# Kernel tuning notes

Measured on AMD Instinct MI355X. Metric: run time of the kernel, lower is better.

## Reference

```python
import jax, jax.numpy as jnp
import numpy as np

GROUP_SIZE = 64


def _ternary_ste(w):
    # bf16 group-wise ternary quantization with straight-through estimator
    wb = w.astype(jnp.bfloat16)
    w_g = wb.reshape(-1, GROUP_SIZE)
    scale = jnp.clip(jnp.mean(jnp.abs(w_g), axis=-1, keepdims=True), 1e-8, None)
    q = (jnp.clip(jnp.round(w_g / scale), -1, 1) * scale).reshape(wb.shape)
    # forward value = q, gradient flows through wb (bf16 cast of w)
    return wb + jax.lax.stop_gradient(q - wb)


def setup_inputs() -> dict:
    key = jax.random.key(0)
    k_x, k_f, k_p = jax.random.split(key, 3)
    N, in_f, out_f, num_f = 16384, 1024, 4096, 16
    x = jax.random.normal(k_x, (N, in_f), dtype=jnp.float32)
    features = jax.random.uniform(k_f, (num_f, in_f), minval=-0.02, maxval=0.02, dtype=jnp.float32)
    prototypes = jax.random.uniform(k_p, (out_f, in_f), minval=-0.02, maxval=0.02, dtype=jnp.float32)
    theta = jnp.float32(1.0)
    alpha = jnp.float32(0.5)
    beta = jnp.float32(0.5)
    return {"x": x, "features": features, "prototypes": prototypes,
            "theta": theta, "alpha": alpha, "beta": beta}


def reference(x, features, prototypes, theta, alpha, beta):
    # low-rank feature projections (K = num_features = 16)
    x_f = x @ features.T                                   # [N, 16]
    p_q = _ternary_ste(prototypes).astype(jnp.float32)     # [out, in]
    p_f = p_q @ features.T                                 # [out, 16]
    x_s = jax.nn.sigmoid(x_f * 5.0)
    p_s = jax.nn.sigmoid(p_f * 5.0)
    x_a = x_f * x_s
    p_a = p_f * p_s
    return (jnp.abs(theta) * (x_a @ p_a.T)
            - jnp.abs(alpha) * (x_a @ (1.0 - p_s).T)
            - jnp.abs(beta) * ((1.0 - x_s) @ p_a.T))
```

## Files before the change

### kernel.cpp

```cpp
#include <hip/hip_runtime.h>
#include <hip/hip_bf16.h>
#include <math.h>

#define NF     16
#define INF    1024
#define NPROTO 4096
#define NROWS  16384

typedef __attribute__((ext_vector_type(8))) short short8;
typedef __attribute__((ext_vector_type(4))) float f32x4;
typedef __attribute__((ext_vector_type(2))) float f32x2;

__device__ __forceinline__ float bf16_rne(float x) {
    unsigned u = __float_as_uint(x);
    unsigned r = (u + 0x7FFFu + ((u >> 16) & 1u)) & 0xFFFF0000u;
    return __uint_as_float(r);
}
__device__ __forceinline__ unsigned short bf16_hi(float v) {
    unsigned u = __float_as_uint(v);
    return (unsigned short)((u + 0x7FFFu + ((u >> 16) & 1u)) >> 16);
}
__device__ __forceinline__ void split_bf16(float v, unsigned short& hi, unsigned short& lo) {
    unsigned u  = __float_as_uint(v);
    unsigned r  = u + 0x7FFFu + ((u >> 16) & 1u);
    hi = (unsigned short)(r >> 16);
    float hf = __uint_as_float(r & 0xFFFF0000u);
    lo = bf16_hi(v - hf);
}
__device__ __forceinline__ float sigmoid5(float z) {
    return 1.0f / (1.0f + __expf(-5.0f * z));
}

__global__ __launch_bounds__(256) void bfrag_kernel(
    const float* __restrict__ feat,
    unsigned short* __restrict__ BFh, unsigned short* __restrict__ BFl)
{
    const int t = blockIdx.x * 256 + threadIdx.x;
    const int kstep = t >> 6, lane = t & 63;
    const int n = lane & 15, b = lane >> 4;
    const float* src = feat + (size_t)n * INF + kstep * 32 + b * 8;
    float4 v0 = *(const float4*)(src);
    float4 v1 = *(const float4*)(src + 4);
    unsigned short h[8], l[8];
    split_bf16(v0.x, h[0], l[0]); split_bf16(v0.y, h[1], l[1]);
    split_bf16(v0.z, h[2], l[2]); split_bf16(v0.w, h[3], l[3]);
    split_bf16(v1.x, h[4], l[4]); split_bf16(v1.y, h[5], l[5]);
    split_bf16(v1.z, h[6], l[6]); split_bf16(v1.w, h[7], l[7]);
#pragma unroll
    for (int e = 0; e < 8; ++e) { BFh[t * 8 + e] = h[e]; BFl[t * 8 + e] = l[e]; }
}

__global__ __launch_bounds__(256, 4) void prep(
    const float* __restrict__ x, const float* __restrict__ proto,
    const float* __restrict__ theta, const float* __restrict__ alpha,
    const float* __restrict__ beta,
    const unsigned short* __restrict__ BFh, const unsigned short* __restrict__ BFl,
    unsigned short* __restrict__ Ph, unsigned short* __restrict__ Pl,
    unsigned short* __restrict__ Xh, unsigned short* __restrict__ Xl)
{
    __shared__ f32x4 red[4][64];
    const int lane = threadIdx.x & 63;
    const int w    = threadIdx.x >> 6;
    const int m = lane & 15, b = lane >> 4;
    const int blk = blockIdx.x;
    const bool is_pe = (blk < NPROTO / 16);
    const int rowbase = (is_pe ? blk : blk - NPROTO / 16) * 16;
    const float* rowp = (is_pe ? proto : x) + (size_t)(rowbase + m) * INF;

    f32x4 acc = {0.f, 0.f, 0.f, 0.f};

    if (is_pe) {
#pragma unroll
        for (int gi = 0; gi < 4; ++gi) {
            const int g = w * 4 + gi;
            const float* pg = rowp + g * 64 + b * 8;
            float4 v0 = *(const float4*)(pg);
            float4 v1 = *(const float4*)(pg + 4);
            float4 v2 = *(const float4*)(pg + 32);
            float4 v3 = *(const float4*)(pg + 36);
            float w0 = bf16_rne(v0.x), w1 = bf16_rne(v0.y), w2 = bf16_rne(v0.z), w3 = bf16_rne(v0.w);
            float w4 = bf16_rne(v1.x), w5 = bf16_rne(v1.y), w6 = bf16_rne(v1.z), w7 = bf16_rne(v1.w);
            float w8 = bf16_rne(v2.x), w9 = bf16_rne(v2.y), wa = bf16_rne(v2.z), wb = bf16_rne(v2.w);
            float wc = bf16_rne(v3.x), wd = bf16_rne(v3.y), we = bf16_rne(v3.z), wf = bf16_rne(v3.w);
            float p0 = ((fabsf(w0) + fabsf(w1)) + fabsf(w2)) + fabsf(w3);
            float p1 = ((fabsf(w4) + fabsf(w5)) + fabsf(w6)) + fabsf(w7);
            float p2 = ((fabsf(w8) + fabsf(w9)) + fabsf(wa)) + fabsf(wb);
            float p3 = ((fabsf(wc) + fabsf(wd)) + fabsf(we)) + fabsf(wf);
            float p = ((p0 + p1) + p2) + p3;
            p += __shfl_xor(p, 16, 64);
            p += __shfl_xor(p, 32, 64);
            float scale = fmaxf(bf16_rne(p * (1.0f / 64.0f)), 1e-8f);
            float inv = 1.0f / scale;
            short8 A0, A1;
            A0[0] = (short)bf16_hi(fminf(fmaxf(rintf(bf16_rne(w0 * inv)), -1.f), 1.f) * scale);
            A0[1] = (short)bf16_hi(fminf(fmaxf(rintf(bf16_rne(w1 * inv)), -1.f), 1.f) * scale);
            A0[2] = (short)bf16_hi(fminf(fmaxf(rintf(bf16_rne(w2 * inv)), -1.f), 1.f) * scale);
            A0[3] = (short)bf16_hi(fminf(fmaxf(rintf(bf16_rne(w3 * inv)), -1.f), 1.f) * scale);
            A0[4] = (short)bf16_hi(fminf(fmaxf(rintf(bf16_rne(w4 * inv)), -1.f), 1.f) * scale);
            A0[5] = (short)bf16_hi(fminf(fmaxf(rintf(bf16_rne(w5 * inv)), -1.f), 1.f) * scale);
            A0[6] = (short)bf16_hi(fminf(fmaxf(rintf(bf16_rne(w6 * inv)), -1.f), 1.f) * scale);
            A0[7] = (short)bf16_hi(fminf(fmaxf(rintf(bf16_rne(w7 * inv)), -1.f), 1.f) * scale);
            A1[0] = (short)bf16_hi(fminf(fmaxf(rintf(bf16_rne(w8 * inv)), -1.f), 1.f) * scale);
            A1[1] = (short)bf16_hi(fminf(fmaxf(rintf(bf16_rne(w9 * inv)), -1.f), 1.f) * scale);
            A1[2] = (short)bf16_hi(fminf(fmaxf(rintf(bf16_rne(wa * inv)), -1.f), 1.f) * scale);
            A1[3] = (short)bf16_hi(fminf(fmaxf(rintf(bf16_rne(wb * inv)), -1.f), 1.f) * scale);
            A1[4] = (short)bf16_hi(fminf(fmaxf(rintf(bf16_rne(wc * inv)), -1.f), 1.f) * scale);
            A1[5] = (short)bf16_hi(fminf(fmaxf(rintf(bf16_rne(wd * inv)), -1.f), 1.f) * scale);
            A1[6] = (short)bf16_hi(fminf(fmaxf(rintf(bf16_rne(we * inv)), -1.f), 1.f) * scale);
            A1[7] = (short)bf16_hi(fminf(fmaxf(rintf(bf16_rne(wf * inv)), -1.f), 1.f) * scale);
            const short8 Bh0 = *(const short8*)(BFh + ((size_t)(2 * g) * 64 + lane) * 8);
            const short8 Bl0 = *(const short8*)(BFl + ((size_t)(2 * g) * 64 + lane) * 8);
            const short8 Bh1 = *(const short8*)(BFh + ((size_t)(2 * g + 1) * 64 + lane) * 8);
            const short8 Bl1 = *(const short8*)(BFl + ((size_t)(2 * g + 1) * 64 + lane) * 8);
            acc = __builtin_amdgcn_mfma_f32_16x16x32_bf16(A0, Bh0, acc, 0, 0, 0);
            acc = __builtin_amdgcn_mfma_f32_16x16x32_bf16(A0, Bl0, acc, 0, 0, 0);
            acc = __builtin_amdgcn_mfma_f32_16x16x32_bf16(A1, Bh1, acc, 0, 0, 0);
            acc = __builtin_amdgcn_mfma_f32_16x16x32_bf16(A1, Bl1, acc, 0, 0, 0);
        }
    } else {
#pragma unroll
        for (int ki = 0; ki < 8; ++ki) {
            const int kstep = w * 8 + ki;
            const float* pk = rowp + kstep * 32 + b * 8;
            float4 v0 = *(const float4*)(pk);
            float4 v1 = *(const float4*)(pk + 4);
            unsigned short h0,l0,h1,l1,h2,l2,h3,l3,h4,l4,h5,l5,h6,l6,h7,l7;
            split_bf16(v0.x, h0, l0); split_bf16(v0.y, h1, l1);
            split_bf16(v0.z, h2, l2); split_bf16(v0.w, h3, l3);
            split_bf16(v1.x, h4, l4); split_bf16(v1.y, h5, l5);
            split_bf16(v1.z, h6, l6); split_bf16(v1.w, h7, l7);
            short8 Ah, Al;
            Ah[0]=(short)h0; Ah[1]=(short)h1; Ah[2]=(short)h2; Ah[3]=(short)h3;
            Ah[4]=(short)h4; Ah[5]=(short)h5; Ah[6]=(short)h6; Ah[7]=(short)h7;
            Al[0]=(short)l0; Al[1]=(short)l1; Al[2]=(short)l2; Al[3]=(short)l3;
            Al[4]=(short)l4; Al[5]=(short)l5; Al[6]=(short)l6; Al[7]=(short)l7;
            const short8 Bh = *(const short8*)(BFh + ((size_t)kstep * 64 + lane) * 8);
            const short8 Bl = *(const short8*)(BFl + ((size_t)kstep * 64 + lane) * 8);
            acc = __builtin_amdgcn_mfma_f32_16x16x32_bf16(Ah, Bh, acc, 0, 0, 0);
            acc = __builtin_amdgcn_mfma_f32_16x16x32_bf16(Ah, Bl, acc, 0, 0, 0);
            acc = __builtin_amdgcn_mfma_f32_16x16x32_bf16(Al, Bh, acc, 0, 0, 0);
            acc = __builtin_amdgcn_mfma_f32_16x16x32_bf16(Al, Bl, acc, 0, 0, 0);
        }
    }

    red[w][lane] = acc;
    __syncthreads();
    if (w == 0) {
        f32x4 a0 = red[0][lane], a1 = red[1][lane], a2 = red[2][lane], a3 = red[3][lane];
        f32x4 tot = (a0 + a1) + (a2 + a3);
        if (is_pe) {
            const float th = fabsf(theta[0]);
            const float al = fabsf(alpha[0]);
            const float be = fabsf(beta[0]);
#pragma unroll
            for (int reg = 0; reg < 4; ++reg) {
                const int row = rowbase + b * 4 + reg;
                float pf = tot[reg];
                float ps = sigmoid5(pf);
                float pa = pf * ps;
                unsigned short h0,l0,h1,l1;
                split_bf16(th * pa - al * (1.0f - ps), h0, l0);
                split_bf16(-be * pa, h1, l1);
                Ph[row * 32 + m]      = h0;  Pl[row * 32 + m]      = l0;
                Ph[row * 32 + 16 + m] = h1;  Pl[row * 32 + 16 + m] = l1;
            }
        } else {
#pragma unroll
            for (int reg = 0; reg < 4; ++reg) {
                const int row = rowbase + b * 4 + reg;
                float xf = tot[reg];
                float xs = sigmoid5(xf);
                unsigned short h0,l0,h1,l1;
                split_bf16(xf * xs, h0, l0);
                split_bf16(1.0f - xs, h1, l1);
                Xh[row * 32 + m]      = h0;  Xl[row * 32 + m]      = l0;
                Xh[row * 32 + 16 + m] = h1;  Xl[row * 32 + 16 + m] = l1;
            }
        }
    }
}

__global__ __launch_bounds__(64) void main_mm_mfma(
    const unsigned short* __restrict__ Xh, const unsigned short* __restrict__ Xl,
    const unsigned short* __restrict__ Ph,
    float* __restrict__ out)
{
    __shared__ float lds[16][128];
    const int lane  = threadIdx.x & 63;
    const int m     = lane & 15;
    const int b     = lane >> 4;
    const int nbase = blockIdx.y * 16;
    const int ob    = blockIdx.x * 128;

    const size_t boff = (size_t)(nbase + m) * 32 + b * 8;
    const short8 Bh = *(const short8*)(Xh + boff);
    const short8 Bl = *(const short8*)(Xl + boff);

    const int wsw = 4 * (m & 7);
    float* myrow = &lds[m][0];
#pragma unroll
    for (int t = 0; t < 8; ++t) {
        const size_t aoff = (size_t)(ob + t * 16 + m) * 32 + b * 8;
        const short8 Ah = *(const short8*)(Ph + aoff);
        f32x4 acc = {0.f, 0.f, 0.f, 0.f};
        acc = __builtin_amdgcn_mfma_f32_16x16x32_bf16(Ah, Bh, acc, 0, 0, 0);
        acc = __builtin_amdgcn_mfma_f32_16x16x32_bf16(Ah, Bl, acc, 0, 0, 0);
        *(f32x4*)(myrow + ((t * 16 + b * 4) ^ wsw)) = acc;
    }

    const float* src = &lds[0][0];
#pragma unroll
    for (int r = 0; r < 16; ++r) {
        f32x2 v = *(const f32x2*)(src + r * 128 + ((lane * 2) ^ (4 * (r & 7))));
        f32x2* dst = (f32x2*)(out + (size_t)(nbase + r) * NPROTO + ob + lane * 2);
        __builtin_nontemporal_store(v, dst);
    }
}

extern "C" void kernel_launch(void* const* d_in, const int* in_sizes, int n_in,
                              void* d_out, int out_size, void* d_ws, size_t ws_size,
                              hipStream_t stream) {
    const float* x     = (const float*)d_in[0];
    const float* feat  = (const float*)d_in[1];
    const float* proto = (const float*)d_in[2];
    const float* theta = (const float*)d_in[3];
    const float* alpha = (const float*)d_in[4];
    const float* beta  = (const float*)d_in[5];
    float* out = (float*)d_out;

    unsigned short* Ph  = (unsigned short*)d_ws;
    unsigned short* Pl  = Ph + (size_t)NPROTO * 32;
    unsigned short* Xh  = Pl + (size_t)NPROTO * 32;
    unsigned short* Xl  = Xh + (size_t)NROWS * 32;
    unsigned short* BFh = Xl + (size_t)NROWS * 32;
    unsigned short* BFl = BFh + (size_t)2048 * 8;

    bfrag_kernel<<<dim3(8), 256, 0, stream>>>(feat, BFh, BFl);
    prep<<<dim3(NPROTO / 16 + NROWS / 16), 256, 0, stream>>>(
        x, proto, theta, alpha, beta, BFh, BFl, Ph, Pl, Xh, Xl);
    main_mm_mfma<<<dim3(NPROTO / 128, NROWS / 16), 64, 0, stream>>>(Xh, Xl, Ph, out);
}
```

Baseline: 69.68 us.

## Fuse x-feature projection into main matmul kernel and split prototype prep

Prototype prep now runs in its own kernel, and the x projection (x@features with hi/lo bf16 split plus sigmoid activation) moves into the main output kernel. The per-row X fragments are staged in LDS instead of going through global workspace. Each 256-thread block then produces a 16x4096 output strip, with its four waves each covering 1024 columns. This removes the Xh/Xl global round trip and one dispatch, at the cost of fewer blocks (1024) each doing much more serial work and using more LDS. The Pl buffer is also dropped, since the main matmul never read it.

```diff
diff --git a/kernel.cpp b/kernel.cpp
--- a/kernel.cpp
+++ b/kernel.cpp
@@ -50,97 +50,67 @@
     for (int e = 0; e < 8; ++e) { BFh[t * 8 + e] = h[e]; BFl[t * 8 + e] = l[e]; }
 }
 
-__global__ __launch_bounds__(256, 4) void prep(
-    const float* __restrict__ x, const float* __restrict__ proto,
+__global__ __launch_bounds__(256, 4) void prep_pe(
+    const float* __restrict__ proto,
     const float* __restrict__ theta, const float* __restrict__ alpha,
     const float* __restrict__ beta,
     const unsigned short* __restrict__ BFh, const unsigned short* __restrict__ BFl,
-    unsigned short* __restrict__ Ph, unsigned short* __restrict__ Pl,
-    unsigned short* __restrict__ Xh, unsigned short* __restrict__ Xl)
+    unsigned short* __restrict__ Ph)
 {
     __shared__ f32x4 red[4][64];
     const int lane = threadIdx.x & 63;
     const int w    = threadIdx.x >> 6;
     const int m = lane & 15, b = lane >> 4;
-    const int blk = blockIdx.x;
-    const bool is_pe = (blk < NPROTO / 16);
-    const int rowbase = (is_pe ? blk : blk - NPROTO / 16) * 16;
-    const float* rowp = (is_pe ? proto : x) + (size_t)(rowbase + m) * INF;
+    const int rowbase = blockIdx.x * 16;
+    const float* rowp = proto + (size_t)(rowbase + m) * INF;
 
     f32x4 acc = {0.f, 0.f, 0.f, 0.f};
-
-    if (is_pe) {
-#pragma unroll
-        for (int gi = 0; gi < 4; ++gi) {
-            const int g = w * 4 + gi;
-            const float* pg = rowp + g * 64 + b * 8;
-            float4 v0 = *(const float4*)(pg);
-            float4 v1 = *(const float4*)(pg + 4);
-            float4 v2 = *(const float4*)(pg + 32);
-            float4 v3 = *(const float4*)(pg + 36);
-            float w0 = bf16_rne(v0.x), w1 = bf16_rne(v0.y), w2 = bf16_rne(v0.z), w3 = bf16_rne(v0.w);
-            float w4 = bf16_rne(v1.x), w5 = bf16_rne(v1.y), w6 = bf16_rne(v1.z), w7 = bf16_rne(v1.w);
-            float w8 = bf16_rne(v2.x), w9 = bf16_rne(v2.y), wa = bf16_rne(v2.z), wb = bf16_rne(v2.w);
-            float wc = bf16_rne(v3.x), wd = bf16_rne(v3.y), we = bf16_rne(v3.z), wf = bf16_rne(v3.w);
-            float p0 = ((fabsf(w0) + fabsf(w1)) + fabsf(w2)) + fabsf(w3);
-            float p1 = ((fabsf(w4) + fabsf(w5)) + fabsf(w6)) + fabsf(w7);
-            float p2 = ((fabsf(w8) + fabsf(w9)) + fabsf(wa)) + fabsf(wb);
-            float p3 = ((fabsf(wc) + fabsf(wd)) + fabsf(we)) + fabsf(wf);
-            float p = ((p0 + p1) + p2) + p3;
-            p += __shfl_xor(p, 16, 64);
-            p += __shfl_xor(p, 32, 64);
-            float scale = fmaxf(bf16_rne(p * (1.0f / 64.0f)), 1e-8f);
-            float inv = 1.0f / scale;
-            short8 A0, A1;
-            A0[0] = (short)bf16_hi(fminf(fmaxf(rintf(bf16_rne(w0 * inv)), -1.f), 1.f) * scale);
-            A0[1] = (short)bf16_hi(fminf(fmaxf(rintf(bf16_rne(w1 * inv)), -1.f), 1.f) * scale);
-            A0[2] = (short)bf16_hi(fminf(fmaxf(rintf(bf16_rne(w2 * inv)), -1.f), 1.f) * scale);
-            A0[3] = (short)bf16_hi(fminf(fmaxf(rintf(bf16_rne(w3 * inv)), -1.f), 1.f) * scale);
-            A0[4] = (short)bf16_hi(fminf(fmaxf(rintf(bf16_rne(w4 * inv)), -1.f), 1.f) * scale);
-            A0[5] = (short)bf16_hi(fminf(fmaxf(rintf(bf16_rne(w5 * inv)), -1.f), 1.f) * scale);
-            A0[6] = (short)bf16_hi(fminf(fmaxf(rintf(bf16_rne(w6 * inv)), -1.f), 1.f) * scale);
-            A0[7] = (short)bf16_hi(fminf(fmaxf(rintf(bf16_rne(w7 * inv)), -1.f), 1.f) * scale);
-            A1[0] = (short)bf16_hi(fminf(fmaxf(rintf(bf16_rne(w8 * inv)), -1.f), 1.f) * scale);
-            A1[1] = (short)bf16_hi(fminf(fmaxf(rintf(bf16_rne(w9 * inv)), -1.f), 1.f) * scale);
-            A1[2] = (short)bf16_hi(fminf(fmaxf(rintf(bf16_rne(wa * inv)), -1.f), 1.f) * scale);
-            A1[3] = (short)bf16_hi(fminf(fmaxf(rintf(bf16_rne(wb * inv)), -1.f), 1.f) * scale);
-            A1[4] = (short)bf16_hi(fminf(fmaxf(rintf(bf16_rne(wc * inv)), -1.f), 1.f) * scale);
-            A1[5] = (short)bf16_hi(fminf(fmaxf(rintf(bf16_rne(wd * inv)), -1.f), 1.f) * scale);
-            A1[6] = (short)bf16_hi(fminf(fmaxf(rintf(bf16_rne(we * inv)), -1.f), 1.f) * scale);
-            A1[7] = (short)bf16_hi(fminf(fmaxf(rintf(bf16_rne(wf * inv)), -1.f), 1.f) * scale);
-            const short8 Bh0 = *(const short8*)(BFh + ((size_t)(2 * g) * 64 + lane) * 8);
-            const short8 Bl0 = *(const short8*)(BFl + ((size_t)(2 * g) * 64 + lane) * 8);
-            const short8 Bh1 = *(const short8*)(BFh + ((size_t)(2 * g + 1) * 64 + lane) * 8);
-            const short8 Bl1 = *(const short8*)(BFl + ((size_t)(2 * g + 1) * 64 + lane) * 8);
-            acc = __builtin_amdgcn_mfma_f32_16x16x32_bf16(A0, Bh0, acc, 0, 0, 0);
-            acc = __builtin_amdgcn_mfma_f32_16x16x32_bf16(A0, Bl0, acc, 0, 0, 0);
-            acc = __builtin_amdgcn_mfma_f32_16x16x32_bf16(A1, Bh1, acc, 0, 0, 0);
-            acc = __builtin_amdgcn_mfma_f32_16x16x32_bf16(A1, Bl1, acc, 0, 0, 0);
-        }
-    } else {
-#pragma unroll
-        for (int ki = 0; ki < 8; ++ki) {
-            const int kstep = w * 8 + ki;
-            const float* pk = rowp + kstep * 32 + b * 8;
-            float4 v0 = *(const float4*)(pk);
-            float4 v1 = *(const float4*)(pk + 4);
-            unsigned short h0,l0,h1,l1,h2,l2,h3,l3,h4,l4,h5,l5,h6,l6,h7,l7;
-            split_bf16(v0.x, h0, l0); split_bf16(v0.y, h1, l1);
-            split_bf16(v0.z, h2, l2); split_bf16(v0.w, h3, l3);
-            split_bf16(v1.x, h4, l4); split_bf16(v1.y, h5, l5);
-            split_bf16(v1.z, h6, l6); split_bf16(v1.w, h7, l7);
-            short8 Ah, Al;
-            Ah[0]=(short)h0; Ah[1]=(short)h1; Ah[2]=(short)h2; Ah[3]=(short)h3;
-            Ah[4]=(short)h4; Ah[5]=(short)h5; Ah[6]=(short)h6; Ah[7]=(short)h7;
-            Al[0]=(short)l0; Al[1]=(short)l1; Al[2]=(short)l2; Al[3]=(short)l3;
-            Al[4]=(short)l4; Al[5]=(short)l5; Al[6]=(short)l6; Al[7]=(short)l7;
-            const short8 Bh = *(const short8*)(BFh + ((size_t)kstep * 64 + lane) * 8);
-            const short8 Bl = *(const short8*)(BFl + ((size_t)kstep * 64 + lane) * 8);
-            acc = __builtin_amdgcn_mfma_f32_16x16x32_bf16(Ah, Bh, acc, 0, 0, 0);
-            acc = __builtin_amdgcn_mfma_f32_16x16x32_bf16(Ah, Bl, acc, 0, 0, 0);
-            acc = __builtin_amdgcn_mfma_f32_16x16x32_bf16(Al, Bh, acc, 0, 0, 0);
-            acc = __builtin_amdgcn_mfma_f32_16x16x32_bf16(Al, Bl, acc, 0, 0, 0);
-        }
+#pragma unroll
+    for (int gi = 0; gi < 4; ++gi) {
+        const int g = w * 4 + gi;
+        const float* pg = rowp + g * 64 + b * 8;
+        float4 v0 = *(const float4*)(pg);
+        float4 v1 = *(const float4*)(pg + 4);
+        float4 v2 = *(const float4*)(pg + 32);
+        float4 v3 = *(const float4*)(pg + 36);
+        float w0 = bf16_rne(v0.x), w1 = bf16_rne(v0.y), w2 = bf16_rne(v0.z), w3 = bf16_rne(v0.w);
+        float w4 = bf16_rne(v1.x), w5 = bf16_rne(v1.y), w6 = bf16_rne(v1.z), w7 = bf16_rne(v1.w);
+        float w8 = bf16_rne(v2.x), w9 = bf16_rne(v2.y), wa = bf16_rne(v2.z), wb = bf16_rne(v2.w);
+        float wc = bf16_rne(v3.x), wd = bf16_rne(v3.y), we = bf16_rne(v3.z), wf = bf16_rne(v3.w);
+        float p0 = ((fabsf(w0) + fabsf(w1)) + fabsf(w2)) + fabsf(w3);
+        float p1 = ((fabsf(w4) + fabsf(w5)) + fabsf(w6)) + fabsf(w7);
+        float p2 = ((fabsf(w8) + fabsf(w9)) + fabsf(wa)) + fabsf(wb);
+        float p3 = ((fabsf(wc) + fabsf(wd)) + fabsf(we)) + fabsf(wf);
+        float p = ((p0 + p1) + p2) + p3;
+        p += __shfl_xor(p, 16, 64);
+        p += __shfl_xor(p, 32, 64);
+        float scale = fmaxf(bf16_rne(p * (1.0f / 64.0f)), 1e-8f);
+        float inv = 1.0f / scale;
+        short8 A0, A1;
+        A0[0] = (short)bf16_hi(fminf(fmaxf(rintf(bf16_rne(w0 * inv)), -1.f), 1.f) * scale);
+        A0[1] = (short)bf16_hi(fminf(fmaxf(rintf(bf16_rne(w1 * inv)), -1.f), 1.f) * scale);
+        A0[2] = (short)bf16_hi(fminf(fmaxf(rintf(bf16_rne(w2 * inv)), -1.f), 1.f) * scale);
+        A0[3] = (short)bf16_hi(fminf(fmaxf(rintf(bf16_rne(w3 * inv)), -1.f), 1.f) * scale);
+        A0[4] = (short)bf16_hi(fminf(fmaxf(rintf(bf16_rne(w4 * inv)), -1.f), 1.f) * scale);
+        A0[5] = (short)bf16_hi(fminf(fmaxf(rintf(bf16_rne(w5 * inv)), -1.f), 1.f) * scale);
+        A0[6] = (short)bf16_hi(fminf(fmaxf(rintf(bf16_rne(w6 * inv)), -1.f), 1.f) * scale);
+        A0[7] = (short)bf16_hi(fminf(fmaxf(rintf(bf16_rne(w7 * inv)), -1.f), 1.f) * scale);
+        A1[0] = (short)bf16_hi(fminf(fmaxf(rintf(bf16_rne(w8 * inv)), -1.f), 1.f) * scale);
+        A1[1] = (short)bf16_hi(fminf(fmaxf(rintf(bf16_rne(w9 * inv)), -1.f), 1.f) * scale);
+        A1[2] = (short)bf16_hi(fminf(fmaxf(rintf(bf16_rne(wa * inv)), -1.f), 1.f) * scale);
+        A1[3] = (short)bf16_hi(fminf(fmaxf(rintf(bf16_rne(wb * inv)), -1.f), 1.f) * scale);
+        A1[4] = (short)bf16_hi(fminf(fmaxf(rintf(bf16_rne(wc * inv)), -1.f), 1.f) * scale);
+        A1[5] = (short)bf16_hi(fminf(fmaxf(rintf(bf16_rne(wd * inv)), -1.f), 1.f) * scale);
+        A1[6] = (short)bf16_hi(fminf(fmaxf(rintf(bf16_rne(we * inv)), -1.f), 1.f) * scale);
+        A1[7] = (short)bf16_hi(fminf(fmaxf(rintf(bf16_rne(wf * inv)), -1.f), 1.f) * scale);
+        const short8 Bh0 = *(const short8*)(BFh + ((size_t)(2 * g) * 64 + lane) * 8);
+        const short8 Bl0 = *(const short8*)(BFl + ((size_t)(2 * g) * 64 + lane) * 8);
+        const short8 Bh1 = *(const short8*)(BFh + ((size_t)(2 * g + 1) * 64 + lane) * 8);
+        const short8 Bl1 = *(const short8*)(BFl + ((size_t)(2 * g + 1) * 64 + lane) * 8);
+        acc = __builtin_amdgcn_mfma_f32_16x16x32_bf16(A0, Bh0, acc, 0, 0, 0);
+        acc = __builtin_amdgcn_mfma_f32_16x16x32_bf16(A0, Bl0, acc, 0, 0, 0);
+        acc = __builtin_amdgcn_mfma_f32_16x16x32_bf16(A1, Bh1, acc, 0, 0, 0);
+        acc = __builtin_amdgcn_mfma_f32_16x16x32_bf16(A1, Bl1, acc, 0, 0, 0);
     }
 
     red[w][lane] = acc;
@@ -148,72 +118,104 @@
     if (w == 0) {
         f32x4 a0 = red[0][lane], a1 = red[1][lane], a2 = red[2][lane], a3 = red[3][lane];
         f32x4 tot = (a0 + a1) + (a2 + a3);
-        if (is_pe) {
-            const float th = fabsf(theta[0]);
-            const float al = fabsf(alpha[0]);
-            const float be = fabsf(beta[0]);
-#pragma unroll
-            for (int reg = 0; reg < 4; ++reg) {
-                const int row = rowbase + b * 4 + reg;
-                float pf = tot[reg];
-                float ps = sigmoid5(pf);
-                float pa = pf * ps;
-                unsigned short h0,l0,h1,l1;
-                split_bf16(th * pa - al * (1.0f - ps), h0, l0);
-                split_bf16(-be * pa, h1, l1);
-                Ph[row * 32 + m]      = h0;  Pl[row * 32 + m]      = l0;
-                Ph[row * 32 + 16 + m] = h1;  Pl[row * 32 + 16 + m] = l1;
-            }
-        } else {
-#pragma unroll
-            for (int reg = 0; reg < 4; ++reg) {
-                const int row = rowbase + b * 4 + reg;
-                float xf = tot[reg];
-                float xs = sigmoid5(xf);
-                unsigned short h0,l0,h1,l1;
-                split_bf16(xf * xs, h0, l0);
-                split_bf16(1.0f - xs, h1, l1);
-                Xh[row * 32 + m]      = h0;  Xl[row * 32 + m]      = l0;
-                Xh[row * 32 + 16 + m] = h1;  Xl[row * 32 + 16 + m] = l1;
-            }
-        }
-    }
-}
-
-__global__ __launch_bounds__(64) void main_mm_mfma(
-    const unsigned short* __restrict__ Xh, const unsigned short* __restrict__ Xl,
+        const float th = fabsf(theta[0]);
+        const float al = fabsf(alpha[0]);
+        const float be = fabsf(beta[0]);
+#pragma unroll
+        for (int reg = 0; reg < 4; ++reg) {
+            const int row = rowbase + b * 4 + reg;
+            float pf = tot[reg];
+            float ps = sigmoid5(pf);
+            float pa = pf * ps;
+            Ph[row * 32 + m]      = bf16_hi(th * pa - al * (1.0f - ps));
+            Ph[row * 32 + 16 + m] = bf16_hi(-be * pa);
+        }
+    }
+}
+
+__global__ __launch_bounds__(256, 4) void fused_main(
+    const float* __restrict__ x,
+    const unsigned short* __restrict__ BFh, const unsigned short* __restrict__ BFl,
     const unsigned short* __restrict__ Ph,
     float* __restrict__ out)
 {
-    __shared__ float lds[16][128];
-    const int lane  = threadIdx.x & 63;
-    const int m     = lane & 15;
-    const int b     = lane >> 4;
-    const int nbase = blockIdx.y * 16;
-    const int ob    = blockIdx.x * 128;
-
-    const size_t boff = (size_t)(nbase + m) * 32 + b * 8;
-    const short8 Bh = *(const short8*)(Xh + boff);
-    const short8 Bl = *(const short8*)(Xl + boff);
-
-    const int wsw = 4 * (m & 7);
-    float* myrow = &lds[m][0];
-#pragma unroll
-    for (int t = 0; t < 8; ++t) {
-        const size_t aoff = (size_t)(ob + t * 16 + m) * 32 + b * 8;
-        const short8 Ah = *(const short8*)(Ph + aoff);
-        f32x4 acc = {0.f, 0.f, 0.f, 0.f};
+    __shared__ float ldsT[4][16][128];
+    __shared__ f32x4 red[4][64];
+    __shared__ unsigned short XeH[16][32], XeL[16][32];
+
+    const int lane = threadIdx.x & 63;
+    const int w    = threadIdx.x >> 6;
+    const int m = lane & 15, b = lane >> 4;
+    const int rowbase = blockIdx.x * 16;
+    const float* rowp = x + (size_t)(rowbase + m) * INF;
+
+    f32x4 acc = {0.f, 0.f, 0.f, 0.f};
+#pragma unroll
+    for (int ki = 0; ki < 8; ++ki) {
+        const int kstep = w * 8 + ki;
+        const float* pk = rowp + kstep * 32 + b * 8;
+        float4 v0 = *(const float4*)(pk);
+        float4 v1 = *(const float4*)(pk + 4);
+        unsigned short h0,l0,h1,l1,h2,l2,h3,l3,h4,l4,h5,l5,h6,l6,h7,l7;
+        split_bf16(v0.x, h0, l0); split_bf16(v0.y, h1, l1);
+        split_bf16(v0.z, h2, l2); split_bf16(v0.w, h3, l3);
+        split_bf16(v1.x, h4, l4); split_bf16(v1.y, h5, l5);
+        split_bf16(v1.z, h6, l6); split_bf16(v1.w, h7, l7);
+        short8 Ah, Al;
+        Ah[0]=(short)h0; Ah[1]=(short)h1; Ah[2]=(short)h2; Ah[3]=(short)h3;
+        Ah[4]=(short)h4; Ah[5]=(short)h5; Ah[6]=(short)h6; Ah[7]=(short)h7;
+        Al[0]=(short)l0; Al[1]=(short)l1; Al[2]=(short)l2; Al[3]=(short)l3;
+        Al[4]=(short)l4; Al[5]=(short)l5; Al[6]=(short)l6; Al[7]=(short)l7;
+        const short8 Bh = *(const short8*)(BFh + ((size_t)kstep * 64 + lane) * 8);
+        const short8 Bl = *(const short8*)(BFl + ((size_t)kstep * 64 + lane) * 8);
         acc = __builtin_amdgcn_mfma_f32_16x16x32_bf16(Ah, Bh, acc, 0, 0, 0);
         acc = __builtin_amdgcn_mfma_f32_16x16x32_bf16(Ah, Bl, acc, 0, 0, 0);
-        *(f32x4*)(myrow + ((t * 16 + b * 4) ^ wsw)) = acc;
-    }
-
-    const float* src = &lds[0][0];
-#pragma unroll
-    for (int r = 0; r < 16; ++r) {
-        f32x2 v = *(const f32x2*)(src + r * 128 + ((lane * 2) ^ (4 * (r & 7))));
-        f32x2* dst = (f32x2*)(out + (size_t)(nbase + r) * NPROTO + ob + lane * 2);
-        __builtin_nontemporal_store(v, dst);
+        acc = __builtin_amdgcn_mfma_f32_16x16x32_bf16(Al, Bh, acc, 0, 0, 0);
+        acc = __builtin_amdgcn_mfma_f32_16x16x32_bf16(Al, Bl, acc, 0, 0, 0);
+    }
+    red[w][lane] = acc;
+    __syncthreads();
+    if (w == 0) {
+        f32x4 a0 = red[0][lane], a1 = red[1][lane], a2 = red[2][lane], a3 = red[3][lane];
+        f32x4 tot = (a0 + a1) + (a2 + a3);
+#pragma unroll
+        for (int reg = 0; reg < 4; ++reg) {
+            const int row = b * 4 + reg;
+            float xf = tot[reg];
+            float xs = sigmoid5(xf);
+            unsigned short h0,l0,h1,l1;
+            split_bf16(xf * xs, h0, l0);
+            split_bf16(1.0f - xs, h1, l1);
+            XeH[row][m]      = h0;  XeL[row][m]      = l0;
+            XeH[row][16 + m] = h1;  XeL[row][16 + m] = l1;
+        }
+    }
+    __syncthreads();
+
+    const short8 Bh = *(const short8*)&XeH[m][b * 8];
+    const short8 Bl = *(const short8*)&XeL[m][b * 8];
+    const int wsw = 4 * (m & 7);
+    float* myrow = &ldsT[w][m][0];
+    const float* src = &ldsT[w][0][0];
+
+#pragma unroll 1
+    for (int c = 0; c < 8; ++c) {
+        const int ob = w * 1024 + c * 128;
+#pragma unroll
+        for (int t = 0; t < 8; ++t) {
+            const size_t aoff = (size_t)(ob + t * 16 + m) * 32 + b * 8;
+            const short8 Ah = *(const short8*)(Ph + aoff);
+            f32x4 a2 = {0.f, 0.f, 0.f, 0.f};
+            a2 = __builtin_amdgcn_mfma_f32_16x16x32_bf16(Ah, Bh, a2, 0, 0, 0);
+            a2 = __builtin_amdgcn_mfma_f32_16x16x32_bf16(Ah, Bl, a2, 0, 0, 0);
+            *(f32x4*)(myrow + ((t * 16 + b * 4) ^ wsw)) = a2;
+        }
+#pragma unroll
+        for (int r = 0; r < 16; ++r) {
+            f32x2 v = *(const f32x2*)(src + r * 128 + ((lane * 2) ^ (4 * (r & 7))));
+            f32x2* dst = (f32x2*)(out + (size_t)(rowbase + r) * NPROTO + ob + lane * 2);
+            __builtin_nontemporal_store(v, dst);
+        }
     }
 }
 
@@ -229,14 +231,10 @@
     float* out = (float*)d_out;
 
     unsigned short* Ph  = (unsigned short*)d_ws;
-    unsigned short* Pl  = Ph + (size_t)NPROTO * 32;
-    unsigned short* Xh  = Pl + (size_t)NPROTO * 32;
-    unsigned short* Xl  = Xh + (size_t)NROWS * 32;
-    unsigned short* BFh = Xl + (size_t)NROWS * 32;
+    unsigned short* BFh = Ph + (size_t)NPROTO * 32;
     unsigned short* BFl = BFh + (size_t)2048 * 8;
 
     bfrag_kernel<<<dim3(8), 256, 0, stream>>>(feat, BFh, BFl);
-    prep<<<dim3(NPROTO / 16 + NROWS / 16), 256, 0, stream>>>(
-        x, proto, theta, alpha, beta, BFh, BFl, Ph, Pl, Xh, Xl);
-    main_mm_mfma<<<dim3(NPROTO / 128, NROWS / 16), 64, 0, stream>>>(Xh, Xl, Ph, out);
-}
+    prep_pe<<<dim3(NPROTO / 16), 256, 0, stream>>>(proto, theta, alpha, beta, BFh, BFl, Ph);
+    fused_main<<<dim3(NROWS / 16), 256, 0, stream>>>(x, BFh, BFl, Ph, out);
+}
```

Result: slower. 74.99 us (+7.6%).

## Widen prep blocks to 8 waves, batch loads, and drop unused Pl buffer

Applied to the files above, without the earlier changes.

The prep kernel now runs 512 threads (8 waves) per block, so each wave handles half as much of the K dimension, and all global loads are issued before any compute to raise memory-level parallelism. The final reduction sums 8 partial accumulators. The prototype low-bf16 part (Pl) is no longer computed or stored, which removes writes the main kernel never read. The risk is lower occupancy per CU from the larger blocks and higher register pressure from the batched loads.

```diff
diff --git a/kernel.cpp b/kernel.cpp
--- a/kernel.cpp
+++ b/kernel.cpp
@@ -50,15 +50,15 @@
     for (int e = 0; e < 8; ++e) { BFh[t * 8 + e] = h[e]; BFl[t * 8 + e] = l[e]; }
 }
 
-__global__ __launch_bounds__(256, 4) void prep(
+__global__ __launch_bounds__(512, 4) void prep(
     const float* __restrict__ x, const float* __restrict__ proto,
     const float* __restrict__ theta, const float* __restrict__ alpha,
     const float* __restrict__ beta,
     const unsigned short* __restrict__ BFh, const unsigned short* __restrict__ BFl,
-    unsigned short* __restrict__ Ph, unsigned short* __restrict__ Pl,
+    unsigned short* __restrict__ Ph,
     unsigned short* __restrict__ Xh, unsigned short* __restrict__ Xl)
 {
-    __shared__ f32x4 red[4][64];
+    __shared__ f32x4 red[8][64];
     const int lane = threadIdx.x & 63;
     const int w    = threadIdx.x >> 6;
     const int m = lane & 15, b = lane >> 4;
@@ -70,18 +70,22 @@
     f32x4 acc = {0.f, 0.f, 0.f, 0.f};
 
     if (is_pe) {
-#pragma unroll
-        for (int gi = 0; gi < 4; ++gi) {
-            const int g = w * 4 + gi;
-            const float* pg = rowp + g * 64 + b * 8;
-            float4 v0 = *(const float4*)(pg);
-            float4 v1 = *(const float4*)(pg + 4);
-            float4 v2 = *(const float4*)(pg + 32);
-            float4 v3 = *(const float4*)(pg + 36);
-            float w0 = bf16_rne(v0.x), w1 = bf16_rne(v0.y), w2 = bf16_rne(v0.z), w3 = bf16_rne(v0.w);
-            float w4 = bf16_rne(v1.x), w5 = bf16_rne(v1.y), w6 = bf16_rne(v1.z), w7 = bf16_rne(v1.w);
-            float w8 = bf16_rne(v2.x), w9 = bf16_rne(v2.y), wa = bf16_rne(v2.z), wb = bf16_rne(v2.w);
-            float wc = bf16_rne(v3.x), wd = bf16_rne(v3.y), we = bf16_rne(v3.z), wf = bf16_rne(v3.w);
+        float4 s[2][4];
+#pragma unroll
+        for (int gi = 0; gi < 2; ++gi) {
+            const float* pg = rowp + (2 * w + gi) * 64 + b * 8;
+            s[gi][0] = *(const float4*)(pg);
+            s[gi][1] = *(const float4*)(pg + 4);
+            s[gi][2] = *(const float4*)(pg + 32);
+            s[gi][3] = *(const float4*)(pg + 36);
+        }
+#pragma unroll
+        for (int gi = 0; gi < 2; ++gi) {
+            const int g = 2 * w + gi;
+            float w0 = bf16_rne(s[gi][0].x), w1 = bf16_rne(s[gi][0].y), w2 = bf16_rne(s[gi][0].z), w3 = bf16_rne(s[gi][0].w);
+            float w4 = bf16_rne(s[gi][1].x), w5 = bf16_rne(s[gi][1].y), w6 = bf16_rne(s[gi][1].z), w7 = bf16_rne(s[gi][1].w);
+            float w8 = bf16_rne(s[gi][2].x), w9 = bf16_rne(s[gi][2].y), wa = bf16_rne(s[gi][2].z), wb = bf16_rne(s[gi][2].w);
+            float wc = bf16_rne(s[gi][3].x), wd = bf16_rne(s[gi][3].y), we = bf16_rne(s[gi][3].z), wf = bf16_rne(s[gi][3].w);
             float p0 = ((fabsf(w0) + fabsf(w1)) + fabsf(w2)) + fabsf(w3);
             float p1 = ((fabsf(w4) + fabsf(w5)) + fabsf(w6)) + fabsf(w7);
             float p2 = ((fabsf(w8) + fabsf(w9)) + fabsf(wa)) + fabsf(wb);
@@ -118,17 +122,21 @@
             acc = __builtin_amdgcn_mfma_f32_16x16x32_bf16(A1, Bl1, acc, 0, 0, 0);
         }
     } else {
-#pragma unroll
-        for (int ki = 0; ki < 8; ++ki) {
-            const int kstep = w * 8 + ki;
-            const float* pk = rowp + kstep * 32 + b * 8;
-            float4 v0 = *(const float4*)(pk);
-            float4 v1 = *(const float4*)(pk + 4);
+        float4 s[4][2];
+#pragma unroll
+        for (int ki = 0; ki < 4; ++ki) {
+            const float* pk = rowp + (4 * w + ki) * 32 + b * 8;
+            s[ki][0] = *(const float4*)(pk);
+            s[ki][1] = *(const float4*)(pk + 4);
+        }
+#pragma unroll
+        for (int ki = 0; ki < 4; ++ki) {
+            const int kstep = 4 * w + ki;
             unsigned short h0,l0,h1,l1,h2,l2,h3,l3,h4,l4,h5,l5,h6,l6,h7,l7;
-            split_bf16(v0.x, h0, l0); split_bf16(v0.y, h1, l1);
-            split_bf16(v0.z, h2, l2); split_bf16(v0.w, h3, l3);
-            split_bf16(v1.x, h4, l4); split_bf16(v1.y, h5, l5);
-            split_bf16(v1.z, h6, l6); split_bf16(v1.w, h7, l7);
+            split_bf16(s[ki][0].x, h0, l0); split_bf16(s[ki][0].y, h1, l1);
+            split_bf16(s[ki][0].z, h2, l2); split_bf16(s[ki][0].w, h3, l3);
+            split_bf16(s[ki][1].x, h4, l4); split_bf16(s[ki][1].y, h5, l5);
+            split_bf16(s[ki][1].z, h6, l6); split_bf16(s[ki][1].w, h7, l7);
             short8 Ah, Al;
             Ah[0]=(short)h0; Ah[1]=(short)h1; Ah[2]=(short)h2; Ah[3]=(short)h3;
             Ah[4]=(short)h4; Ah[5]=(short)h5; Ah[6]=(short)h6; Ah[7]=(short)h7;
@@ -146,8 +154,9 @@
     red[w][lane] = acc;
     __syncthreads();
     if (w == 0) {
-        f32x4 a0 = red[0][lane], a1 = red[1][lane], a2 = red[2][lane], a3 = red[3][lane];
-        f32x4 tot = (a0 + a1) + (a2 + a3);
+        f32x4 t0 = (red[0][lane] + red[1][lane]) + (red[2][lane] + red[3][lane]);
+        f32x4 t1 = (red[4][lane] + red[5][lane]) + (red[6][lane] + red[7][lane]);
+        f32x4 tot = t0 + t1;
         if (is_pe) {
             const float th = fabsf(theta[0]);
             const float al = fabsf(alpha[0]);
@@ -158,11 +167,8 @@
                 float pf = tot[reg];
                 float ps = sigmoid5(pf);
                 float pa = pf * ps;
-                unsigned short h0,l0,h1,l1;
-                split_bf16(th * pa - al * (1.0f - ps), h0, l0);
-                split_bf16(-be * pa, h1, l1);
-                Ph[row * 32 + m]      = h0;  Pl[row * 32 + m]      = l0;
-                Ph[row * 32 + 16 + m] = h1;  Pl[row * 32 + 16 + m] = l1;
+                Ph[row * 32 + m]      = bf16_hi(th * pa - al * (1.0f - ps));
+                Ph[row * 32 + 16 + m] = bf16_hi(-be * pa);
             }
         } else {
 #pragma unroll
@@ -229,14 +235,13 @@
     float* out = (float*)d_out;
 
     unsigned short* Ph  = (unsigned short*)d_ws;
-    unsigned short* Pl  = Ph + (size_t)NPROTO * 32;
-    unsigned short* Xh  = Pl + (size_t)NPROTO * 32;
+    unsigned short* Xh  = Ph + (size_t)NPROTO * 32;
     unsigned short* Xl  = Xh + (size_t)NROWS * 32;
     unsigned short* BFh = Xl + (size_t)NROWS * 32;
     unsigned short* BFl = BFh + (size_t)2048 * 8;
 
     bfrag_kernel<<<dim3(8), 256, 0, stream>>>(feat, BFh, BFl);
-    prep<<<dim3(NPROTO / 16 + NROWS / 16), 256, 0, stream>>>(
-        x, proto, theta, alpha, beta, BFh, BFl, Ph, Pl, Xh, Xl);
+    prep<<<dim3(NPROTO / 16 + NROWS / 16), 512, 0, stream>>>(
+        x, proto, theta, alpha, beta, BFh, BFl, Ph, Xh, Xl);
     main_mm_mfma<<<dim3(NPROTO / 128, NROWS / 16), 64, 0, stream>>>(Xh, Xl, Ph, out);
 }
```

Measured after the change: 70.72 us. About the same (+1.5%).
